# Performance work log

Hardware: AMD Instinct MI355X
Metric: run time of the kernel (lower is better)

Reference implementation:

```python
import jax, jax.numpy as jnp
import numpy as np

# Gemma config constants (layer_idx=0 -> 'sliding_attention')
H = 8          # num query heads
KVH = 4        # num kv heads
DH = 256       # head_dim
SW = 1024      # sliding_window
ROPE_BASE = 10000.0   # rope_local_base_freq (sliding layer)
EPS = 1e-6
SCALE = 256.0 ** -0.5  # query_pre_attn_scalar ** -0.5


def _rms_norm(x, w):
    # Gemma RMSNorm: fp32 norm, scale by (1 + w)
    x32 = x.astype(jnp.float32)
    n = x32 * jax.lax.rsqrt(jnp.mean(x32 * x32, axis=-1, keepdims=True) + EPS)
    return (n * (1.0 + w.astype(jnp.float32))).astype(x.dtype)


def _rope_cos_sin(S):
    inv_freq = 1.0 / (ROPE_BASE ** (jnp.arange(0, DH, 2, dtype=jnp.float32) / DH))
    freqs = jnp.outer(jnp.arange(S, dtype=jnp.float32), inv_freq)  # [S, DH/2]
    emb = jnp.concatenate([freqs, freqs], axis=-1)                 # [S, DH]
    return jnp.cos(emb), jnp.sin(emb)


def _rotate_half(x):
    x1, x2 = jnp.split(x, 2, axis=-1)
    return jnp.concatenate([-x2, x1], axis=-1)


def _apply_rope(x, cos, sin):
    # x: [B, H, S, DH]; cos/sin: [S, DH]
    return x * cos[None, None] + _rotate_half(x) * sin[None, None]


def setup_inputs() -> dict:
    key = jax.random.key(0)
    ks = jax.random.split(key, 7)
    B, S, D = 2, 2048, 2048
    w = lambda k, shape: jax.random.normal(k, shape, jnp.float32) * 0.02
    return {
        "hidden_states": jax.random.normal(ks[0], (B, S, D), jnp.float32),
        "Wq": w(ks[1], (H * DH, D)),
        "Wk": w(ks[2], (KVH * DH, D)),
        "Wv": w(ks[3], (KVH * DH, D)),
        "Wo": w(ks[4], (D, H * DH)),
        "q_norm_w": jnp.zeros((DH,), jnp.float32),
        "k_norm_w": jnp.zeros((DH,), jnp.float32),
    }


def reference(hidden_states, Wq, Wk, Wv, Wo, q_norm_w, k_norm_w):
    B, S, D = hidden_states.shape
    # projections (no bias)
    q = jnp.einsum("bsd,ed->bse", hidden_states, Wq).reshape(B, S, H, DH).transpose(0, 2, 1, 3)
    k = jnp.einsum("bsd,ed->bse", hidden_states, Wk).reshape(B, S, KVH, DH).transpose(0, 2, 1, 3)
    v = jnp.einsum("bsd,ed->bse", hidden_states, Wv).reshape(B, S, KVH, DH).transpose(0, 2, 1, 3)
    # Gemma q/k RMSNorm over head_dim, then RoPE (local base for sliding layer)
    q = _rms_norm(q, q_norm_w)
    k = _rms_norm(k, k_norm_w)
    cos, sin = _rope_cos_sin(S)
    q = _apply_rope(q, cos, sin)
    k = _apply_rope(k, cos, sin)
    # GQA: repeat kv heads
    rep = H // KVH
    k = jnp.repeat(k, rep, axis=1)
    v = jnp.repeat(v, rep, axis=1)
    # causal sliding-window mask
    i = jnp.arange(S)[:, None]
    j = jnp.arange(S)[None, :]
    mask = (j <= i) & (i - j < SW)  # [S, S]
    scores = jnp.einsum("bhqd,bhkd->bhqk", q, k) * SCALE
    scores = jnp.where(mask[None, None], scores, jnp.finfo(jnp.float32).min)
    attn = jax.nn.softmax(scores.astype(jnp.float32), axis=-1).astype(q.dtype)
    out = jnp.einsum("bhqk,bhkd->bhqd", attn, v)  # [B, H, S, DH]
    out = out.transpose(0, 2, 1, 3).reshape(B, S, H * DH)
    return jnp.einsum("bse,de->bsd", out, Wo)
```

## Files before the change

kernel.cpp:

```cpp
#include <hip/hip_runtime.h>
#include <hip/hip_bf16.h>


typedef __bf16 bf16x8 __attribute__((ext_vector_type(8)));
typedef __bf16 bf16x4 __attribute__((ext_vector_type(4)));
typedef float f32x4 __attribute__((ext_vector_type(4)));

#define NB 2
#define SEQ 2048
#define DMODEL 2048
#define NH 8
#define NKV 4
#define DHEAD 256
#define SWIN 1024

#define AS1 __attribute__((address_space(1)))
#define AS3 __attribute__((address_space(3)))

static __device__ __forceinline__ void gload_lds16(const void* g, void* l) {
    __builtin_amdgcn_global_load_lds((const AS1 void*)g, (AS3 void*)l, 16, 0, 0);
}

static __device__ __forceinline__ bf16x4 tr16(const __bf16* p) {
    bf16x4 r;
    asm volatile("ds_read_b64_tr_b16 %0, %1" : "=v"(r) : "v"((const AS3 __bf16*)p));
    return r;
}

__global__ void cvt_rope(const float* __restrict__ s0, const float* __restrict__ s1,
                         const float* __restrict__ s2, const float* __restrict__ s3,
                         const float* __restrict__ s4, __bf16* __restrict__ d0,
                         __bf16* __restrict__ d1, __bf16* __restrict__ d2,
                         __bf16* __restrict__ d3, __bf16* __restrict__ d4,
                         float* __restrict__ cosT, float* __restrict__ sinT) {
    if (blockIdx.x >= 20480) {
        int idx = (blockIdx.x - 20480) * 256 + threadIdx.x;
        int s = idx >> 7, i = idx & 127;
        float fr = (float)s * __expf(-(float)i * 0.0719557843f);
        cosT[idx] = cosf(fr);
        sinT[idx] = sinf(fr);
        return;
    }
    int i = blockIdx.x * 256 + threadIdx.x;
    const float* src; __bf16* dst;
    if (i < 2097152) { src = s0; dst = d0; }
    else if (i < 3145728) { i -= 2097152; src = s1; dst = d1; }
    else if (i < 3670016) { i -= 3145728; src = s2; dst = d2; }
    else if (i < 4194304) { i -= 3670016; src = s3; dst = d3; }
    else                  { i -= 4194304; src = s4; dst = d4; }
    f32x4 v = ((const f32x4*)src)[i];
    bf16x4 o;
#pragma unroll
    for (int j = 0; j < 4; ++j) o[j] = (__bf16)v[j];
    ((bf16x4*)dst)[i] = o;
}

template <int OUTBF16>
__global__ __launch_bounds__(512, 2)
void gemm_bt8(const __bf16* __restrict__ A, const __bf16* __restrict__ B,
              void* __restrict__ Cv, int M, int N, int K, int nbx) {
    __shared__ __align__(16) __bf16 sA[2][256 * 64];
    __shared__ __align__(16) __bf16 sB[2][256 * 64];
    const int tid = threadIdx.x;
    const int wave = tid >> 6, lane = tid & 63;
    const int lo = lane & 15, hi = lane >> 4;
    const int wm = wave >> 2, wn = wave & 3;
    const int qq = (int)gridDim.x >> 3;
    const int swz = ((int)blockIdx.x & 7) * qq + ((int)blockIdx.x >> 3);
    const int bx = swz % nbx, by = swz / nbx;
    const int brow = by * 256, bcol = bx * 256;
    const int xr = lo & 7;

    int aoff[4];
#pragma unroll
    for (int i = 0; i < 4; ++i) {
        int n = i * 512 + tid, r = n >> 3, s = n & 7;
        aoff[i] = r * K + ((s ^ (r & 7)) << 3);
    }
    const __bf16* Ab = A + (size_t)brow * K;
    const __bf16* Bb = B + (size_t)bcol * K;

    auto stgA = [&](int bsel, int kt, int h) {
        const __bf16* ga = Ab + kt * 64;
#pragma unroll
        for (int ii = 0; ii < 2; ++ii) {
            int i = h + ii * 2;
            gload_lds16(ga + aoff[i], (char*)&sA[bsel][0] + (i * 512 + wave * 64) * 16);
        }
    };
    auto stgB = [&](int bsel, int kt, int h) {
        const __bf16* gb = Bb + kt * 64;
#pragma unroll
        for (int i = 2 * h; i < 2 * h + 2; ++i)
            gload_lds16(gb + aoff[i], (char*)&sB[bsel][0] + (i * 512 + wave * 64) * 16);
    };

    f32x4 acc[8][4] = {};
    const int nt = K >> 6;

    stgA(0, 0, 0); stgA(0, 0, 1); stgB(0, 0, 0); stgB(0, 0, 1);
    stgA(1, 1, 0); stgA(1, 1, 1); stgB(1, 1, 0); stgB(1, 1, 1);
    asm volatile("s_waitcnt vmcnt(8)" ::: "memory");
    __builtin_amdgcn_s_barrier();

    for (int t = 0; t < nt; ++t) {
        const int buf = t & 1;
        const bool pre = (t + 2 < nt);
        const __bf16* sa = &sA[buf][0];
        const __bf16* sb = &sB[buf][0];
        bf16x8 af[8], b0[4], b1[4];
#pragma unroll
        for (int m = 0; m < 4; ++m)
#pragma unroll
            for (int ks = 0; ks < 2; ++ks)
                af[m * 2 + ks] = *(const bf16x8*)&sa[(wm * 128 + m * 16 + lo) * 64 + (((ks * 4 + hi) ^ xr) << 3)];
#pragma unroll
        for (int n = 0; n < 2; ++n)
#pragma unroll
            for (int ks = 0; ks < 2; ++ks)
                b0[n * 2 + ks] = *(const bf16x8*)&sb[(wn * 64 + n * 16 + lo) * 64 + (((ks * 4 + hi) ^ xr) << 3)];
        __builtin_amdgcn_sched_barrier(0);
        __builtin_amdgcn_s_barrier();
        __builtin_amdgcn_s_setprio(1);
#pragma unroll
        for (int m = 0; m < 4; ++m)
#pragma unroll
            for (int n = 0; n < 2; ++n)
#pragma unroll
                for (int ks = 0; ks < 2; ++ks)
                    acc[m][n] = __builtin_amdgcn_mfma_f32_16x16x32_bf16(af[m * 2 + ks], b0[n * 2 + ks], acc[m][n], 0, 0, 0);
        __builtin_amdgcn_s_setprio(0);
        __builtin_amdgcn_sched_barrier(0);
        __builtin_amdgcn_s_barrier();
#pragma unroll
        for (int n = 0; n < 2; ++n)
#pragma unroll
            for (int ks = 0; ks < 2; ++ks)
                b1[n * 2 + ks] = *(const bf16x8*)&sb[(wn * 64 + (n + 2) * 16 + lo) * 64 + (((ks * 4 + hi) ^ xr) << 3)];
        if (pre) stgA(buf, t + 2, 0);
        __builtin_amdgcn_sched_barrier(0);
        __builtin_amdgcn_s_barrier();
        __builtin_amdgcn_s_setprio(1);
#pragma unroll
        for (int m = 0; m < 4; ++m)
#pragma unroll
            for (int n = 0; n < 2; ++n)
#pragma unroll
                for (int ks = 0; ks < 2; ++ks)
                    acc[m][n + 2] = __builtin_amdgcn_mfma_f32_16x16x32_bf16(af[m * 2 + ks], b1[n * 2 + ks], acc[m][n + 2], 0, 0, 0);
        __builtin_amdgcn_s_setprio(0);
        __builtin_amdgcn_sched_barrier(0);
        __builtin_amdgcn_s_barrier();
#pragma unroll
        for (int m = 0; m < 4; ++m)
#pragma unroll
            for (int ks = 0; ks < 2; ++ks)
                af[m * 2 + ks] = *(const bf16x8*)&sa[(wm * 128 + (m + 4) * 16 + lo) * 64 + (((ks * 4 + hi) ^ xr) << 3)];
        if (pre) stgB(buf, t + 2, 1);
        __builtin_amdgcn_sched_barrier(0);
        __builtin_amdgcn_s_barrier();
        __builtin_amdgcn_s_setprio(1);
#pragma unroll
        for (int m = 0; m < 4; ++m)
#pragma unroll
            for (int n = 0; n < 2; ++n)
#pragma unroll
                for (int ks = 0; ks < 2; ++ks)
                    acc[m + 4][n + 2] = __builtin_amdgcn_mfma_f32_16x16x32_bf16(af[m * 2 + ks], b1[n * 2 + ks], acc[m + 4][n + 2], 0, 0, 0);
        __builtin_amdgcn_s_setprio(0);
        __builtin_amdgcn_sched_barrier(0);
        __builtin_amdgcn_s_barrier();
        if (pre) { stgA(buf, t + 2, 1); stgB(buf, t + 2, 0); }
        __builtin_amdgcn_sched_barrier(0);
        __builtin_amdgcn_s_setprio(1);
#pragma unroll
        for (int m = 0; m < 4; ++m)
#pragma unroll
            for (int n = 0; n < 2; ++n)
#pragma unroll
                for (int ks = 0; ks < 2; ++ks)
                    acc[m + 4][n] = __builtin_amdgcn_mfma_f32_16x16x32_bf16(af[m * 2 + ks], b0[n * 2 + ks], acc[m + 4][n], 0, 0, 0);
        __builtin_amdgcn_s_setprio(0);
        if (pre) asm volatile("s_waitcnt vmcnt(8)" ::: "memory");
        else     asm volatile("s_waitcnt vmcnt(0)" ::: "memory");
        __builtin_amdgcn_sched_barrier(0);
        __builtin_amdgcn_s_barrier();
    }

#pragma unroll
    for (int m = 0; m < 8; ++m) {
        int row = brow + wm * 128 + m * 16 + hi * 4;
#pragma unroll
        for (int n = 0; n < 4; ++n) {
            int col = bcol + wn * 64 + n * 16 + lo;
            if constexpr (OUTBF16) {
                __bf16* cp = (__bf16*)Cv + (size_t)row * N + col;
#pragma unroll
                for (int j = 0; j < 4; ++j)
                    cp[(size_t)j * N] = (__bf16)acc[m][n][j];
            } else {
                float* cp = (float*)Cv + (size_t)row * N + col;
#pragma unroll
                for (int j = 0; j < 4; ++j)
                    cp[(size_t)j * N] = acc[m][n][j];
            }
        }
    }
}

__global__ __launch_bounds__(512, 2)
void gemm_bt8n(const __bf16* __restrict__ A, const __bf16* __restrict__ B,
               float* __restrict__ C, int M, int N, int K, int nbx) {
    __shared__ __align__(16) __bf16 sA[2][256 * 64];
    __shared__ __align__(16) __bf16 sB[2][128 * 64];
    const int tid = threadIdx.x;
    const int wave = tid >> 6, lane = tid & 63;
    const int lo = lane & 15, hi = lane >> 4;
    const int wm = wave >> 1, wn = wave & 1;
    const int qq = (int)gridDim.x >> 3;
    const int swz = ((int)blockIdx.x & 7) * qq + ((int)blockIdx.x >> 3);
    const int bx = swz % nbx, by = swz / nbx;
    const int brow = by * 256, bcol = bx * 128;
    const int xr = lo & 7;

    int aoff[4], boff[2];
#pragma unroll
    for (int i = 0; i < 4; ++i) {
        int n = i * 512 + tid, r = n >> 3, s = n & 7;
        aoff[i] = r * K + ((s ^ (r & 7)) << 3);
    }
#pragma unroll
    for (int i = 0; i < 2; ++i) {
        int n = i * 512 + tid, r = n >> 3, s = n & 7;
        boff[i] = r * K + ((s ^ (r & 7)) << 3);
    }
    const __bf16* Ab = A + (size_t)brow * K;
    const __bf16* Bb = B + (size_t)bcol * K;

    auto stgAall = [&](int bsel, int kt) {
        const __bf16* ga = Ab + kt * 64;
#pragma unroll
        for (int i = 0; i < 4; ++i)
            gload_lds16(ga + aoff[i], (char*)&sA[bsel][0] + (i * 512 + wave * 64) * 16);
    };
    auto stgBall = [&](int bsel, int kt) {
        const __bf16* gb = Bb + kt * 64;
#pragma unroll
        for (int i = 0; i < 2; ++i)
            gload_lds16(gb + boff[i], (char*)&sB[bsel][0] + (i * 512 + wave * 64) * 16);
    };

    f32x4 acc[4][4] = {};
    const int nt = K >> 6;

    stgAall(0, 0); stgBall(0, 0);
    stgAall(1, 1); stgBall(1, 1);
    asm volatile("s_waitcnt vmcnt(6)" ::: "memory");
    __builtin_amdgcn_s_barrier();

    for (int t = 0; t < nt; ++t) {
        const int buf = t & 1;
        const bool pre = (t + 2 < nt);
        const __bf16* sa = &sA[buf][0];
        const __bf16* sb = &sB[buf][0];
        bf16x8 af[4], b0[4], b1[4];
#pragma unroll
        for (int m = 0; m < 2; ++m)
#pragma unroll
            for (int ks = 0; ks < 2; ++ks)
                af[m * 2 + ks] = *(const bf16x8*)&sa[(wm * 64 + m * 16 + lo) * 64 + (((ks * 4 + hi) ^ xr) << 3)];
#pragma unroll
        for (int n = 0; n < 2; ++n)
#pragma unroll
            for (int ks = 0; ks < 2; ++ks)
                b0[n * 2 + ks] = *(const bf16x8*)&sb[(wn * 64 + n * 16 + lo) * 64 + (((ks * 4 + hi) ^ xr) << 3)];
        __builtin_amdgcn_sched_barrier(0);
        __builtin_amdgcn_s_barrier();
        __builtin_amdgcn_s_setprio(1);
#pragma unroll
        for (int m = 0; m < 2; ++m)
#pragma unroll
            for (int n = 0; n < 2; ++n)
#pragma unroll
                for (int ks = 0; ks < 2; ++ks)
                    acc[m][n] = __builtin_amdgcn_mfma_f32_16x16x32_bf16(af[m * 2 + ks], b0[n * 2 + ks], acc[m][n], 0, 0, 0);
        __builtin_amdgcn_s_setprio(0);
        __builtin_amdgcn_sched_barrier(0);
        __builtin_amdgcn_s_barrier();
#pragma unroll
        for (int n = 0; n < 2; ++n)
#pragma unroll
            for (int ks = 0; ks < 2; ++ks)
                b1[n * 2 + ks] = *(const bf16x8*)&sb[(wn * 64 + (n + 2) * 16 + lo) * 64 + (((ks * 4 + hi) ^ xr) << 3)];
        __builtin_amdgcn_sched_barrier(0);
        __builtin_amdgcn_s_barrier();
        __builtin_amdgcn_s_setprio(1);
#pragma unroll
        for (int m = 0; m < 2; ++m)
#pragma unroll
            for (int n = 0; n < 2; ++n)
#pragma unroll
                for (int ks = 0; ks < 2; ++ks)
                    acc[m][n + 2] = __builtin_amdgcn_mfma_f32_16x16x32_bf16(af[m * 2 + ks], b1[n * 2 + ks], acc[m][n + 2], 0, 0, 0);
        __builtin_amdgcn_s_setprio(0);
        __builtin_amdgcn_sched_barrier(0);
        __builtin_amdgcn_s_barrier();
#pragma unroll
        for (int m = 0; m < 2; ++m)
#pragma unroll
            for (int ks = 0; ks < 2; ++ks)
                af[m * 2 + ks] = *(const bf16x8*)&sa[(wm * 64 + (m + 2) * 16 + lo) * 64 + (((ks * 4 + hi) ^ xr) << 3)];
        if (pre) stgBall(buf, t + 2);
        __builtin_amdgcn_sched_barrier(0);
        __builtin_amdgcn_s_barrier();
        __builtin_amdgcn_s_setprio(1);
#pragma unroll
        for (int m = 0; m < 2; ++m)
#pragma unroll
            for (int n = 0; n < 2; ++n)
#pragma unroll
                for (int ks = 0; ks < 2; ++ks)
                    acc[m + 2][n + 2] = __builtin_amdgcn_mfma_f32_16x16x32_bf16(af[m * 2 + ks], b1[n * 2 + ks], acc[m + 2][n + 2], 0, 0, 0);
        __builtin_amdgcn_s_setprio(0);
        __builtin_amdgcn_sched_barrier(0);
        __builtin_amdgcn_s_barrier();
        if (pre) stgAall(buf, t + 2);
        __builtin_amdgcn_sched_barrier(0);
        __builtin_amdgcn_s_setprio(1);
#pragma unroll
        for (int m = 0; m < 2; ++m)
#pragma unroll
            for (int n = 0; n < 2; ++n)
#pragma unroll
                for (int ks = 0; ks < 2; ++ks)
                    acc[m + 2][n] = __builtin_amdgcn_mfma_f32_16x16x32_bf16(af[m * 2 + ks], b0[n * 2 + ks], acc[m + 2][n], 0, 0, 0);
        __builtin_amdgcn_s_setprio(0);
        if (pre) asm volatile("s_waitcnt vmcnt(6)" ::: "memory");
        else     asm volatile("s_waitcnt vmcnt(0)" ::: "memory");
        __builtin_amdgcn_sched_barrier(0);
        __builtin_amdgcn_s_barrier();
    }

#pragma unroll
    for (int m = 0; m < 4; ++m) {
        int row = brow + wm * 64 + m * 16 + hi * 4;
#pragma unroll
        for (int n = 0; n < 4; ++n) {
            float* cp = C + (size_t)row * N + bcol + wn * 64 + n * 16 + lo;
#pragma unroll
            for (int j = 0; j < 4; ++j)
                cp[(size_t)j * N] = acc[m][n][j];
        }
    }
}

__global__ __launch_bounds__(256)
void norm_rope(const __bf16* __restrict__ QKV, const float* __restrict__ qw,
               const float* __restrict__ kw, const float* __restrict__ cosT,
               const float* __restrict__ sinT, __bf16* __restrict__ Qo,
               __bf16* __restrict__ Ko, __bf16* __restrict__ Vo) {
    const int r = blockIdx.x;
    const int b = r >> 11, s = r & (SEQ - 1);
    const int wave = threadIdx.x >> 6, lane = threadIdx.x & 63;
    f32x4 cos4 = *(const f32x4*)&cosT[s * 128 + (lane & 31) * 4];
    f32x4 sin4 = *(const f32x4*)&sinT[s * 128 + (lane & 31) * 4];
#pragma unroll
    for (int ii = 0; ii < 4; ++ii) {
        int hh = wave + ii * 4;
        if (hh < 12) {
            bool isq = hh < 8;
            int col0 = isq ? hh * DHEAD : DMODEL + (hh - 8) * DHEAD;
            const __bf16* src = QKV + (size_t)r * 4096 + col0;
            bf16x4 xb = *(const bf16x4*)&src[lane * 4];
            float x[4];
#pragma unroll
            for (int j = 0; j < 4; ++j) x[j] = (float)xb[j];
            float ss = x[0] * x[0] + x[1] * x[1] + x[2] * x[2] + x[3] * x[3];
#pragma unroll
            for (int d2 = 1; d2 < 64; d2 <<= 1) ss += __shfl_xor(ss, d2);
            float scale = rsqrtf(ss * (1.f / DHEAD) + 1e-6f);
            const float* wp = isq ? qw : kw;
            float nx[4];
#pragma unroll
            for (int j = 0; j < 4; ++j)
                nx[j] = x[j] * scale * (1.f + wp[lane * 4 + j]);
            bf16x4 ov;
#pragma unroll
            for (int j = 0; j < 4; ++j) {
                float other = __shfl_xor(nx[j], 32);
                float rot = (lane < 32) ? -other : other;
                float v = nx[j] * cos4[j] + rot * sin4[j];
                if (isq) v *= 0.0625f;
                ov[j] = (__bf16)v;
            }
            __bf16* dst = isq ? (Qo + ((size_t)(b * NH + hh) * SEQ + s) * DHEAD)
                              : (Ko + ((size_t)(b * NKV + (hh - 8)) * SEQ + s) * DHEAD);
            *(bf16x4*)&dst[lane * 4] = ov;
        } else {
            int vh = hh - 12;
            const __bf16* src = QKV + (size_t)r * 4096 + 3072 + vh * DHEAD;
            bf16x4 xb = *(const bf16x4*)&src[lane * 4];
            __bf16* dst = Vo + ((size_t)(b * NKV + vh) * SEQ + s) * DHEAD;
            *(bf16x4*)&dst[lane * 4] = xb;
        }
    }
}

__global__ __launch_bounds__(256)
void attn6(const __bf16* __restrict__ Q, const __bf16* __restrict__ Kb,
           const __bf16* __restrict__ Vb, __bf16* __restrict__ ctx) {
    const int bid = blockIdx.x;
    const int bk = bid & 7;
    const int qt = 63 - (bid >> 3);
    const int b = bk >> 2, kh = bk & 3;
    const int q0 = qt * 32;
    const int tid = threadIdx.x;
    const int wave = tid >> 6, lane = tid & 63;
    const int lo = lane & 15, hi = lane >> 4;
    const int hsel = wave >> 1, qsub = wave & 1;
    const int h = kh * 2 + hsel;
    const int qbase = q0 + qsub * 16;
    const int q = qbase + lo;

    __shared__ __align__(16) __bf16 kbuf[2][32 * 256];
    __shared__ __align__(16) __bf16 vbuf[32 * 256];

    const __bf16* Qp = Q + ((size_t)(b * NH + h) * SEQ + qbase) * DHEAD;
    const __bf16* Kp = Kb + (size_t)(b * NKV + kh) * SEQ * DHEAD;
    const __bf16* Vp = Vb + (size_t)(b * NKV + kh) * SEQ * DHEAD;

    int koff[4], voff[4];
#pragma unroll
    for (int i = 0; i < 4; ++i) {
        int n = i * 256 + tid;
        int r = n >> 5, c = n & 31;
        koff[i] = r * 256 + ((c ^ (r & 7)) << 3);
        int st = n >> 3, w = n & 7;
        int vk = (st & 7) * 4 + (w >> 1);
        int vd = (st >> 3) * 16 + (w & 1) * 8;
        voff[i] = vk * 256 + vd;
    }

    auto stageK = [&](int bsel, int c0) {
        const __bf16* kg = Kp + (size_t)c0 * DHEAD;
        char* kd = (char*)&kbuf[bsel][0] + wave * 1024;
#pragma unroll
        for (int i = 0; i < 4; ++i) gload_lds16(kg + koff[i], kd + i * 4096);
    };
    auto stageV = [&](int c0) {
        const __bf16* vg = Vp + (size_t)c0 * DHEAD;
        char* vd = (char*)&vbuf[0] + wave * 1024;
#pragma unroll
        for (int i = 0; i < 4; ++i) gload_lds16(vg + voff[i], vd + i * 4096);
    };

    bf16x8 qf[8];
#pragma unroll
    for (int dc = 0; dc < 8; ++dc)
        qf[dc] = *(const bf16x8*)(Qp + (size_t)lo * DHEAD + dc * 32 + hi * 8);

    f32x4 o[16] = {};
    float m = -3e38f, l = 0.f;

    int kstart = q0 - SWIN; if (kstart < 0) kstart = 0;
    const int nt = (q0 + 32 - kstart) >> 5;

    stageK(0, kstart);
    asm volatile("s_waitcnt vmcnt(0)" ::: "memory");
    int buf = 0;
    for (int t = 0; t < nt; ++t) {
        const int c0 = kstart + t * 32;
        const bool pre = (t + 1 < nt);
        stageV(c0);
        if (pre) stageK(buf ^ 1, c0 + 32);
        if (pre) asm volatile("s_waitcnt vmcnt(8)" ::: "memory");
        else     asm volatile("s_waitcnt vmcnt(4)" ::: "memory");
        __builtin_amdgcn_sched_barrier(0);
        __builtin_amdgcn_s_barrier();
        __builtin_amdgcn_sched_barrier(0);

        f32x4 sc0 = {}, sc1 = {};
        const __bf16* kb0 = &kbuf[buf][0];
        __builtin_amdgcn_s_setprio(1);
#pragma unroll
        for (int dc = 0; dc < 8; ++dc) {
            int u = dc * 4 + hi;
            bf16x8 kfa = *(const bf16x8*)&kb0[lo * 256 + ((u ^ (lo & 7)) << 3)];
            bf16x8 kfb = *(const bf16x8*)&kb0[(16 + lo) * 256 + ((u ^ ((16 + lo) & 7)) << 3)];
            sc0 = __builtin_amdgcn_mfma_f32_16x16x32_bf16(kfa, qf[dc], sc0, 0, 0, 0);
            sc1 = __builtin_amdgcn_mfma_f32_16x16x32_bf16(kfb, qf[dc], sc1, 0, 0, 0);
        }
        __builtin_amdgcn_s_setprio(0);

        float s8[8];
#pragma unroll
        for (int j = 0; j < 4; ++j) {
            int ka = c0 + hi * 4 + j;
            int kb2 = ka + 16;
            s8[j]     = (ka <= q && q - ka < SWIN) ? sc0[j] : -1e30f;
            s8[4 + j] = (kb2 <= q && q - kb2 < SWIN) ? sc1[j] : -1e30f;
        }
        float pm = s8[0];
#pragma unroll
        for (int i = 1; i < 8; ++i) pm = fmaxf(pm, s8[i]);
        pm = fmaxf(pm, __shfl_xor(pm, 16));
        pm = fmaxf(pm, __shfl_xor(pm, 32));
        if (__any(pm > m + 8.f)) {
            float mn = fmaxf(m, pm);
            float corr = __expf(m - mn);
            l *= corr;
#pragma unroll
            for (int dt = 0; dt < 16; ++dt) o[dt] *= corr;
            m = mn;
        }
        float p8[8], ps = 0.f;
#pragma unroll
        for (int i = 0; i < 8; ++i) {
            float e = __expf(s8[i] - m);
            p8[i] = (s8[i] > -9e29f) ? e : 0.f;
            ps += p8[i];
        }
        ps += __shfl_xor(ps, 16);
        ps += __shfl_xor(ps, 32);
        l += ps;

        bf16x8 paf;
#pragma unroll
        for (int i = 0; i < 8; ++i) paf[i] = (__bf16)p8[i];

        if (pre) asm volatile("s_waitcnt vmcnt(4)" ::: "memory");
        else     asm volatile("s_waitcnt vmcnt(0)" ::: "memory");
        __builtin_amdgcn_sched_barrier(0);
        __builtin_amdgcn_s_barrier();
        __builtin_amdgcn_sched_barrier(0);

        const __bf16* vb0 = &vbuf[0];
#pragma unroll
        for (int dq = 0; dq < 4; ++dq) {
            bf16x4 t0[4], t1[4];
#pragma unroll
            for (int u = 0; u < 4; ++u) {
                int dt = dq * 4 + u;
                t0[u] = tr16(vb0 + (dt * 8 + hi) * 64 + lo * 4);
                t1[u] = tr16(vb0 + (dt * 8 + 4 + hi) * 64 + lo * 4);
            }
            asm volatile("s_waitcnt lgkmcnt(0)" ::: "memory");
            __builtin_amdgcn_sched_barrier(0);
            __builtin_amdgcn_s_setprio(1);
#pragma unroll
            for (int u = 0; u < 4; ++u) {
                bf16x8 vf;
#pragma unroll
                for (int j = 0; j < 4; ++j) { vf[j] = t0[u][j]; vf[4 + j] = t1[u][j]; }
                o[dq * 4 + u] = __builtin_amdgcn_mfma_f32_16x16x32_bf16(vf, paf, o[dq * 4 + u], 0, 0, 0);
            }
            __builtin_amdgcn_s_setprio(0);
        }
        __builtin_amdgcn_sched_barrier(0);
        __builtin_amdgcn_s_barrier();
        __builtin_amdgcn_sched_barrier(0);
        buf ^= 1;
    }

    const float invl = 1.0f / l;
    __bf16* cp = ctx + ((size_t)(b * SEQ + q)) * (NH * DHEAD) + h * DHEAD;
#pragma unroll
    for (int dt = 0; dt < 16; ++dt) {
        bf16x4 w;
#pragma unroll
        for (int j = 0; j < 4; ++j) w[j] = (__bf16)(o[dt][j] * invl);
        *(bf16x4*)&cp[dt * 16 + hi * 4] = w;
    }
}

extern "C" void kernel_launch(void* const* d_in, const int* in_sizes, int n_in,
                              void* d_out, int out_size, void* d_ws, size_t ws_size,
                              hipStream_t stream) {
    const float* hs = (const float*)d_in[0];
    const float* Wq = (const float*)d_in[1];
    const float* Wk = (const float*)d_in[2];
    const float* Wv = (const float*)d_in[3];
    const float* Wo = (const float*)d_in[4];
    const float* qw = (const float*)d_in[5];
    const float* kw = (const float*)d_in[6];
    float* out = (float*)d_out;

    char* ws = (char*)d_ws;
    size_t off = 0;
    auto alloc = [&](size_t bytes) {
        char* p = ws + off;
        off += (bytes + 255) & ~(size_t)255;
        return p;
    };
    const int M = NB * SEQ;
    __bf16* hsB   = (__bf16*)alloc((size_t)M * DMODEL * 2);
    __bf16* WqkvB = (__bf16*)alloc((size_t)4096 * DMODEL * 2);
    __bf16* WoB   = (__bf16*)alloc((size_t)DMODEL * DMODEL * 2);
    __bf16* QKVb  = (__bf16*)alloc((size_t)M * 4096 * 2);
    __bf16* Qb    = (__bf16*)alloc((size_t)M * 2048 * 2);
    __bf16* Kbf   = (__bf16*)alloc((size_t)M * 1024 * 2);
    __bf16* Vbf   = (__bf16*)alloc((size_t)M * 1024 * 2);
    float*  cosT  = (float*) alloc((size_t)SEQ * 128 * 4);
    float*  sinT  = (float*) alloc((size_t)SEQ * 128 * 4);
    __bf16* ctxB  = QKVb;

    cvt_rope<<<21504, 256, 0, stream>>>(hs, Wq, Wk, Wv, Wo,
                                        hsB, WqkvB, WqkvB + (size_t)2048 * 2048,
                                        WqkvB + (size_t)3072 * 2048, WoB, cosT, sinT);

    gemm_bt8<1><<<256, 512, 0, stream>>>(hsB, WqkvB, QKVb, M, 4096, DMODEL, 16);

    norm_rope<<<M, 256, 0, stream>>>(QKVb, qw, kw, cosT, sinT, Qb, Kbf, Vbf);

    attn6<<<512, 256, 0, stream>>>(Qb, Kbf, Vbf, ctxB);

    gemm_bt8n<<<256, 512, 0, stream>>>(ctxB, WoB, out, M, DMODEL, DMODEL, 16);
}
```

Measured before the change: 205.7 us.

## Double-buffer V in attention and prefetch K/V together, one barrier per tile

The attention kernel now keeps two LDS buffers for V as well as K and loads the next tile's K and V together at the start of each iteration. The three block barriers per tile become a single barrier at the end, after waiting for the prefetch. This removes the V load from the critical path between softmax and the PV matmul and cuts synchronisation. In exchange LDS use grows to 64KB per block, which may lower occupancy.

```diff
diff --git a/kernel.cpp b/kernel.cpp
--- a/kernel.cpp
+++ b/kernel.cpp
@@ -407,7 +407,7 @@
 }
 
 __global__ __launch_bounds__(256)
-void attn6(const __bf16* __restrict__ Q, const __bf16* __restrict__ Kb,
+void attn7(const __bf16* __restrict__ Q, const __bf16* __restrict__ Kb,
            const __bf16* __restrict__ Vb, __bf16* __restrict__ ctx) {
     const int bid = blockIdx.x;
     const int bk = bid & 7;
@@ -423,7 +423,7 @@
     const int q = qbase + lo;
 
     __shared__ __align__(16) __bf16 kbuf[2][32 * 256];
-    __shared__ __align__(16) __bf16 vbuf[32 * 256];
+    __shared__ __align__(16) __bf16 vbuf[2][32 * 256];
 
     const __bf16* Qp = Q + ((size_t)(b * NH + h) * SEQ + qbase) * DHEAD;
     const __bf16* Kp = Kb + (size_t)(b * NKV + kh) * SEQ * DHEAD;
@@ -441,17 +441,16 @@
         voff[i] = vk * 256 + vd;
     }
 
-    auto stageK = [&](int bsel, int c0) {
+    auto stage = [&](int bsel, int c0) {
         const __bf16* kg = Kp + (size_t)c0 * DHEAD;
+        const __bf16* vg = Vp + (size_t)c0 * DHEAD;
         char* kd = (char*)&kbuf[bsel][0] + wave * 1024;
-#pragma unroll
-        for (int i = 0; i < 4; ++i) gload_lds16(kg + koff[i], kd + i * 4096);
-    };
-    auto stageV = [&](int c0) {
-        const __bf16* vg = Vp + (size_t)c0 * DHEAD;
-        char* vd = (char*)&vbuf[0] + wave * 1024;
-#pragma unroll
-        for (int i = 0; i < 4; ++i) gload_lds16(vg + voff[i], vd + i * 4096);
+        char* vd = (char*)&vbuf[bsel][0] + wave * 1024;
+#pragma unroll
+        for (int i = 0; i < 4; ++i) {
+            gload_lds16(kg + koff[i], kd + i * 4096);
+            gload_lds16(vg + voff[i], vd + i * 4096);
+        }
     };
 
     bf16x8 qf[8];
@@ -465,19 +464,17 @@
     int kstart = q0 - SWIN; if (kstart < 0) kstart = 0;
     const int nt = (q0 + 32 - kstart) >> 5;
 
-    stageK(0, kstart);
+    stage(0, kstart);
     asm volatile("s_waitcnt vmcnt(0)" ::: "memory");
-    int buf = 0;
+    __builtin_amdgcn_sched_barrier(0);
+    __builtin_amdgcn_s_barrier();
+    __builtin_amdgcn_sched_barrier(0);
+
     for (int t = 0; t < nt; ++t) {
         const int c0 = kstart + t * 32;
+        const int buf = t & 1;
         const bool pre = (t + 1 < nt);
-        stageV(c0);
-        if (pre) stageK(buf ^ 1, c0 + 32);
-        if (pre) asm volatile("s_waitcnt vmcnt(8)" ::: "memory");
-        else     asm volatile("s_waitcnt vmcnt(4)" ::: "memory");
-        __builtin_amdgcn_sched_barrier(0);
-        __builtin_amdgcn_s_barrier();
-        __builtin_amdgcn_sched_barrier(0);
+        if (pre) stage(buf ^ 1, c0 + 32);
 
         f32x4 sc0 = {}, sc1 = {};
         const __bf16* kb0 = &kbuf[buf][0];
@@ -528,13 +525,7 @@
 #pragma unroll
         for (int i = 0; i < 8; ++i) paf[i] = (__bf16)p8[i];
 
-        if (pre) asm volatile("s_waitcnt vmcnt(4)" ::: "memory");
-        else     asm volatile("s_waitcnt vmcnt(0)" ::: "memory");
-        __builtin_amdgcn_sched_barrier(0);
-        __builtin_amdgcn_s_barrier();
-        __builtin_amdgcn_sched_barrier(0);
-
-        const __bf16* vb0 = &vbuf[0];
+        const __bf16* vb0 = &vbuf[buf][0];
 #pragma unroll
         for (int dq = 0; dq < 4; ++dq) {
             bf16x4 t0[4], t1[4];
@@ -556,10 +547,13 @@
             }
             __builtin_amdgcn_s_setprio(0);
         }
-        __builtin_amdgcn_sched_barrier(0);
-        __builtin_amdgcn_s_barrier();
-        __builtin_amdgcn_sched_barrier(0);
-        buf ^= 1;
+
+        if (pre) {
+            asm volatile("s_waitcnt vmcnt(0)" ::: "memory");
+            __builtin_amdgcn_sched_barrier(0);
+            __builtin_amdgcn_s_barrier();
+            __builtin_amdgcn_sched_barrier(0);
+        }
     }
 
     const float invl = 1.0f / l;
@@ -612,7 +606,7 @@
 
     norm_rope<<<M, 256, 0, stream>>>(QKVb, qw, kw, cosT, sinT, Qb, Kbf, Vbf);
 
-    attn6<<<512, 256, 0, stream>>>(Qb, Kbf, Vbf, ctxB);
+    attn7<<<512, 256, 0, stream>>>(Qb, Kbf, Vbf, ctxB);
 
     gemm_bt8n<<<256, 512, 0, stream>>>(ctxB, WoB, out, M, DMODEL, DMODEL, 16);
 }
```

Result: slower. 213.2 us (+3.6%).
